# Kernel optimization log

Hardware: AMD Instinct MI355X
Metric: run time of the kernel (lower is better)

## Reference

```python
import jax, jax.numpy as jnp
import numpy as np

D_MODEL, D_INNER, D_STATE, D_CONV, DT_RANK = 192, 384, 16, 4, 12
EPS = 1e-5


def _causal_dwconv(x, w, b):
    # x: (B, L, Din); w: (Din, 1, K) depthwise; causal left pad K-1
    xc = x.transpose(0, 2, 1)  # (B, Din, L)
    y = jax.lax.conv_general_dilated(xc, w, window_strides=(1,),
                                     padding=[(D_CONV - 1, 0)],
                                     feature_group_count=D_INNER,
                                     dimension_numbers=('NCH', 'OIH', 'NCH'))
    return (y + b[None, :, None]).transpose(0, 2, 1)  # (B, L, Din)


def _ssm_dir(xh, z, conv_w, conv_b, x_proj_w, dt_w, dt_b, A_log, D):
    # one direction of the selective scan
    x = jax.nn.silu(_causal_dwconv(xh, conv_w, conv_b))  # (B, L, Din)
    x_dbl = jnp.einsum('bld,ed->ble', x, x_proj_w)       # (B, L, R+2N)
    dt = jax.nn.softplus(jnp.einsum('blr,dr->bld', x_dbl[..., :DT_RANK], dt_w) + dt_b)
    Bm = x_dbl[..., DT_RANK:DT_RANK + D_STATE]           # (B, L, N)
    Cm = x_dbl[..., DT_RANK + D_STATE:]                  # (B, L, N)
    A = -jnp.exp(A_log)                                  # (Din, N)
    deltaA = jnp.exp(dt[..., None] * A)                  # (B, L, Din, N)
    dBx = (dt * x)[..., None] * Bm[:, :, None, :]        # (B, L, Din, N)

    def comb(e1, e2):
        a1, b1 = e1
        a2, b2 = e2
        return a1 * a2, a2 * b1 + b2

    _, h = jax.lax.associative_scan(comb, (deltaA, dBx), axis=1)
    y = jnp.einsum('bldn,bln->bld', h, Cm) + x * D
    return y * jax.nn.silu(z)


def setup_inputs() -> dict:
    key = jax.random.key(0)
    ks = jax.random.split(key, 24)
    B, L = 2, 2048
    s = 0.02
    inp = {
        'hidden_states': jax.random.normal(ks[0], (B, L, D_MODEL), jnp.float32),
        'residual': jax.random.normal(ks[1], (B, L, D_MODEL), jnp.float32),
        'norm_w': jnp.ones((D_MODEL,), jnp.float32),
        'in_proj_w': jax.random.normal(ks[2], (2 * D_INNER, D_MODEL)) * s,
        'out_proj_w': jax.random.normal(ks[3], (D_MODEL, D_INNER)) * s,
        # forward-direction SSM params
        'conv_w_f': jax.random.normal(ks[4], (D_INNER, 1, D_CONV)) * s,
        'conv_b_f': jnp.zeros((D_INNER,), jnp.float32),
        'x_proj_w_f': jax.random.normal(ks[5], (DT_RANK + 2 * D_STATE, D_INNER)) * s,
        'dt_w_f': jax.random.normal(ks[6], (D_INNER, DT_RANK)) * s,
        'dt_b_f': jax.random.uniform(ks[7], (D_INNER,), minval=-4.0, maxval=-2.0),
        'A_log_f': jnp.log(jnp.tile(jnp.arange(1, D_STATE + 1, dtype=jnp.float32), (D_INNER, 1))),
        'D_f': jnp.ones((D_INNER,), jnp.float32),
        # backward-direction SSM params (bimamba)
        'conv_w_b': jax.random.normal(ks[8], (D_INNER, 1, D_CONV)) * s,
        'conv_b_b': jnp.zeros((D_INNER,), jnp.float32),
        'x_proj_w_b': jax.random.normal(ks[9], (DT_RANK + 2 * D_STATE, D_INNER)) * s,
        'dt_w_b': jax.random.normal(ks[10], (D_INNER, DT_RANK)) * s,
        'dt_b_b': jax.random.uniform(ks[11], (D_INNER,), minval=-4.0, maxval=-2.0),
        'A_log_b': jnp.log(jnp.tile(jnp.arange(1, D_STATE + 1, dtype=jnp.float32), (D_INNER, 1))),
        'D_b': jnp.ones((D_INNER,), jnp.float32),
    }
    return inp


def reference(hidden_states, residual, norm_w, in_proj_w, out_proj_w,
              conv_w_f, conv_b_f, x_proj_w_f, dt_w_f, dt_b_f, A_log_f, D_f,
              conv_w_b, conv_b_b, x_proj_w_b, dt_w_b, dt_b_b, A_log_b, D_b):
    # fused add + RMSNorm (prenorm=True): residual_out = hidden + residual (fp32)
    residual_out = (hidden_states + residual).astype(jnp.float32)
    x = residual_out * jax.lax.rsqrt(jnp.mean(residual_out * residual_out, axis=-1, keepdims=True) + EPS)
    x = x * norm_w
    # Mamba mixer, bimamba=True
    xz = jnp.einsum('bld,ed->ble', x, in_proj_w)  # (B, L, 2*Din)
    xh, z = xz[..., :D_INNER], xz[..., D_INNER:]
    y_f = _ssm_dir(xh, z, conv_w_f, conv_b_f, x_proj_w_f, dt_w_f, dt_b_f, A_log_f, D_f)
    y_b = _ssm_dir(xh[:, ::-1], z[:, ::-1], conv_w_b, conv_b_b, x_proj_w_b, dt_w_b, dt_b_b, A_log_b, D_b)[:, ::-1]
    out = jnp.einsum('bld,ed->ble', y_f + y_b, out_proj_w)
    return out, residual_out
```

## Files before the change

kernel.cpp:

```cpp
#include <hip/hip_runtime.h>
#include <math.h>

#define BB 2
#define LL 2048
#define DM 192
#define DI 384
#define DS 16
#define RK 12
#define NROW (BB*LL)
#define NCH 64
#define CLEN (LL/NCH)
#define EP 48

__device__ __forceinline__ float siluf(float v) { return v / (1.f + __expf(-v)); }

#define N_IN  (DM * 2 * DI)
#define N_OUT (DI * DM)
#define N_XP  (2 * DI * EP)
#define N_DT  (2 * RK * DI)
#define N_PREP (N_IN + N_OUT + N_XP + N_DT)

__global__ __launch_bounds__(256) void k_wprep(
    const float* __restrict__ wip, const float* __restrict__ wop,
    const float* __restrict__ xpwf, const float* __restrict__ xpwb,
    const float* __restrict__ dtwf, const float* __restrict__ dtwb,
    float* __restrict__ wt_in, float* __restrict__ wt_out,
    float* __restrict__ wt_xp, float* __restrict__ wt_dt) {
  int i = blockIdx.x * 256 + threadIdx.x;
  if (i < N_IN) {
    int k = i / (2 * DI), c = i % (2 * DI);
    wt_in[i] = wip[c * DM + k];
  } else if (i < N_IN + N_OUT) {
    int t = i - N_IN;
    int k = t / DM, c = t % DM;
    wt_out[t] = wop[c * DI + k];
  } else if (i < N_IN + N_OUT + N_XP) {
    int t = i - N_IN - N_OUT;
    int dir = t / (DI * EP), rem = t % (DI * EP);
    int k = rem / EP, e = rem % EP;
    const float* src = dir ? xpwb : xpwf;
    wt_xp[t] = (e < RK + 2 * DS) ? src[e * DI + k] : 0.f;
  } else if (i < N_PREP) {
    int t = i - N_IN - N_OUT - N_XP;
    int dir = t / (RK * DI), rem = t % (RK * DI);
    int j = rem / DI, d = rem % DI;
    const float* src = dir ? dtwb : dtwf;
    wt_dt[t] = src[d * RK + j];
  }
}

__global__ __launch_bounds__(256) void k_rmsnorm(
    const float* __restrict__ h, const float* __restrict__ r,
    const float* __restrict__ w, float* __restrict__ res, float* __restrict__ xn) {
  int row = blockIdx.x * 4 + (threadIdx.x >> 6);
  int lane = threadIdx.x & 63;
  const float* hp = h + row * DM;
  const float* rp = r + row * DM;
  float v0 = hp[lane]       + rp[lane];
  float v1 = hp[lane + 64]  + rp[lane + 64];
  float v2 = hp[lane + 128] + rp[lane + 128];
  float ss = v0 * v0 + v1 * v1 + v2 * v2;
  #pragma unroll
  for (int o = 32; o; o >>= 1) ss += __shfl_xor(ss, o);
  float inv = rsqrtf(ss * (1.f / DM) + 1e-5f);
  float* rr = res + row * DM;
  float* xo = xn + row * DM;
  rr[lane] = v0; rr[lane + 64] = v1; rr[lane + 128] = v2;
  xo[lane]       = v0 * inv * w[lane];
  xo[lane + 64]  = v1 * inv * w[lane + 64];
  xo[lane + 128] = v2 * inv * w[lane + 128];
}

__global__ __launch_bounds__(256) void k_inproj(
    const float* __restrict__ xn, const float* __restrict__ wt,
    float* __restrict__ xh, float* __restrict__ z) {
  __shared__ float xs[DM][16];
  int r0 = blockIdx.x * 16;
  int c = blockIdx.y * 256 + threadIdx.x;
  for (int idx = threadIdx.x; idx < 16 * DM; idx += 256) {
    int r = idx & 15, k = idx >> 4;
    xs[k][r] = xn[(r0 + r) * DM + k];
  }
  __syncthreads();
  const float* wc = wt + c;
  float acc[16];
  #pragma unroll
  for (int i = 0; i < 16; i++) acc[i] = 0.f;
  for (int k = 0; k < DM; k += 4) {
    float w0 = wc[(k+0) * (2*DI)];
    float w1 = wc[(k+1) * (2*DI)];
    float w2 = wc[(k+2) * (2*DI)];
    float w3 = wc[(k+3) * (2*DI)];
    float wv4[4] = {w0, w1, w2, w3};
    #pragma unroll
    for (int kk = 0; kk < 4; kk++) {
      float wv = wv4[kk];
      const float4* xr = reinterpret_cast<const float4*>(&xs[k + kk][0]);
      #pragma unroll
      for (int q = 0; q < 4; q++) {
        float4 a = xr[q];
        acc[4*q+0] += wv * a.x; acc[4*q+1] += wv * a.y;
        acc[4*q+2] += wv * a.z; acc[4*q+3] += wv * a.w;
      }
    }
  }
  float* dst = (c < DI) ? (xh + c) : (z + (c - DI));
  #pragma unroll
  for (int r2 = 0; r2 < 16; r2++) dst[(r0 + r2) * DI] = acc[r2];
}

__global__ __launch_bounds__(256) void k_conv(
    const float* __restrict__ xh,
    const float* __restrict__ cwf, const float* __restrict__ cbf,
    const float* __restrict__ cwb, const float* __restrict__ cbb,
    float* __restrict__ xc) {
  int dir = blockIdx.y;
  int g = blockIdx.x * 256 + threadIdx.x;
  int row = g / DI, d = g % DI;
  int b = row >> 11, s = row & (LL - 1);
  const float* cw = dir ? cwb : cwf;
  const float* cb = dir ? cbb : cbf;
  float acc = cb[d];
  #pragma unroll
  for (int k = 0; k < 4; k++) {
    int sp = s - 3 + k;
    if (sp >= 0) {
      int mr = b * LL + (dir ? (LL - 1 - sp) : sp);
      acc += cw[d * 4 + k] * xh[mr * DI + d];
    }
  }
  xc[(dir * NROW + row) * DI + d] = siluf(acc);
}

__global__ __launch_bounds__(256) void k_xproj(
    const float* __restrict__ xc,
    const float* __restrict__ wt_xp, const float* __restrict__ wt_dt,
    const float* __restrict__ dtbf, const float* __restrict__ dtbb,
    float* __restrict__ dt, float* __restrict__ Bm, float* __restrict__ Cm) {
  int dir = blockIdx.y;
  int r0 = blockIdx.x * 16;
  const float* wxp = wt_xp + dir * DI * EP;
  const float* wdt = wt_dt + dir * RK * DI;
  const float* dtb = dir ? dtbb : dtbf;
  __shared__ float xs[16][DI];
  __shared__ float xd[16][EP];
  for (int idx = threadIdx.x; idx < 16 * DI; idx += 256) {
    int r = idx / DI, d2 = idx % DI;
    xs[r][d2] = xc[(size_t)(dir * NROW + r0 + r) * DI + d2];
  }
  __syncthreads();
  for (int o = threadIdx.x; o < 16 * EP; o += 256) {
    int r = o / EP, e = o % EP;
    const float* wcol = wxp + e;
    const float4* xr = reinterpret_cast<const float4*>(&xs[r][0]);
    float ax = 0.f, ay = 0.f, az = 0.f, aw = 0.f;
    #pragma unroll 4
    for (int q = 0; q < DI / 4; q++) {
      float4 x = xr[q];
      ax += wcol[(4*q+0) * EP] * x.x;
      ay += wcol[(4*q+1) * EP] * x.y;
      az += wcol[(4*q+2) * EP] * x.z;
      aw += wcol[(4*q+3) * EP] * x.w;
    }
    xd[r][e] = (ax + ay) + (az + aw);
  }
  __syncthreads();
  for (int o = threadIdx.x; o < 16 * DI; o += 256) {
    int r = o / DI, d2 = o % DI;
    float a = dtb[d2];
    #pragma unroll
    for (int j = 0; j < RK; j++) a += xd[r][j] * wdt[j * DI + d2];
    a = (a > 20.f) ? a : log1pf(__expf(a));
    dt[(size_t)(dir * NROW + r0 + r) * DI + d2] = a;
  }
  for (int o = threadIdx.x; o < 16 * 32; o += 256) {
    int r = o / 32, j = o % 32;
    float v = xd[r][RK + j];
    if (j < DS) Bm[(size_t)(dir * NROW + r0 + r) * DS + j] = v;
    else        Cm[(size_t)(dir * NROW + r0 + r) * DS + (j - DS)] = v;
  }
}

__global__ __launch_bounds__(128) void k_scan1(
    const float* __restrict__ dt, const float* __restrict__ xc,
    const float* __restrict__ Bm,
    const float* __restrict__ Alf, const float* __restrict__ Alb,
    float* __restrict__ S, float* __restrict__ P) {
  int zb = blockIdx.z;
  int dir = zb >> 1;
  int d = blockIdx.x * 128 + threadIdx.x;
  int c = blockIdx.y;
  const float* Al = dir ? Alb : Alf;
  float Av[DS];
  {
    const float4* ap = reinterpret_cast<const float4*>(Al + d * DS);
    #pragma unroll
    for (int q = 0; q < 4; q++) {
      float4 a = ap[q];
      Av[4*q+0] = -__expf(a.x); Av[4*q+1] = -__expf(a.y);
      Av[4*q+2] = -__expf(a.z); Av[4*q+3] = -__expf(a.w);
    }
  }
  int rowbase = zb * LL + c * CLEN;
  const float4* Bp4 = reinterpret_cast<const float4*>(Bm + (size_t)rowbase * DS);
  float h[DS];
  #pragma unroll
  for (int n = 0; n < DS; n++) h[n] = 0.f;
  float sdt = 0.f;
  float dtv = dt[(size_t)rowbase * DI + d];
  float xv  = xc[(size_t)rowbase * DI + d];
  #pragma unroll 4
  for (int s = 0; s < CLEN; s++) {
    float dtn_ = 0.f, xn_ = 0.f;
    if (s + 1 < CLEN) {
      dtn_ = dt[(size_t)(rowbase + s + 1) * DI + d];
      xn_  = xc[(size_t)(rowbase + s + 1) * DI + d];
    }
    float4 B0 = Bp4[s*4+0], B1 = Bp4[s*4+1], B2 = Bp4[s*4+2], B3 = Bp4[s*4+3];
    float Bv[DS] = {B0.x,B0.y,B0.z,B0.w, B1.x,B1.y,B1.z,B1.w,
                    B2.x,B2.y,B2.z,B2.w, B3.x,B3.y,B3.z,B3.w};
    float dtx = dtv * xv;
    sdt += dtv;
    #pragma unroll
    for (int n = 0; n < DS; n++) {
      float dA = __expf(dtv * Av[n]);
      h[n] = __fmaf_rn(dA, h[n], dtx * Bv[n]);
    }
    dtv = dtn_; xv = xn_;
  }
  size_t base = ((size_t)(zb * NCH + c) * DI + d) * DS;
  float4* Sp = reinterpret_cast<float4*>(S + base);
  float4* Pp = reinterpret_cast<float4*>(P + base);
  #pragma unroll
  for (int q = 0; q < 4; q++) {
    Sp[q] = make_float4(h[4*q+0], h[4*q+1], h[4*q+2], h[4*q+3]);
    Pp[q] = make_float4(__expf(Av[4*q+0]*sdt), __expf(Av[4*q+1]*sdt),
                        __expf(Av[4*q+2]*sdt), __expf(Av[4*q+3]*sdt));
  }
}

__global__ __launch_bounds__(256) void k_scan2(
    float* __restrict__ S, const float* __restrict__ P) {
  int g = blockIdx.x * 256 + threadIdx.x;
  int zb = g / (DI * DS);
  int rem = g % (DI * DS);
  const int stride = DI * DS;
  size_t base = (size_t)zb * NCH * stride + rem;
  float carry = 0.f;
  for (int c0 = 0; c0 < NCH; c0 += 8) {
    float p8[8], s8[8];
    #pragma unroll
    for (int j = 0; j < 8; j++) {
      p8[j] = P[base + (size_t)(c0 + j) * stride];
      s8[j] = S[base + (size_t)(c0 + j) * stride];
    }
    #pragma unroll
    for (int j = 0; j < 8; j++) {
      S[base + (size_t)(c0 + j) * stride] = carry;
      carry = __fmaf_rn(p8[j], carry, s8[j]);
    }
  }
}

__global__ __launch_bounds__(128) void k_scan3(
    const float* __restrict__ dt, const float* __restrict__ xc,
    const float* __restrict__ Bm, const float* __restrict__ Cm,
    const float* __restrict__ z, const float* __restrict__ Hin,
    const float* __restrict__ Alf, const float* __restrict__ Alb,
    const float* __restrict__ Df, const float* __restrict__ Db,
    float* __restrict__ y) {
  int zb = blockIdx.z;
  int dir = zb >> 1, b = zb & 1;
  int d = blockIdx.x * 128 + threadIdx.x;
  int c = blockIdx.y;
  const float* Al = dir ? Alb : Alf;
  const float* Dp = dir ? Db : Df;
  float Av[DS];
  {
    const float4* ap = reinterpret_cast<const float4*>(Al + d * DS);
    #pragma unroll
    for (int q = 0; q < 4; q++) {
      float4 a = ap[q];
      Av[4*q+0] = -__expf(a.x); Av[4*q+1] = -__expf(a.y);
      Av[4*q+2] = -__expf(a.z); Av[4*q+3] = -__expf(a.w);
    }
  }
  float Dv = Dp[d];
  int rowbase = zb * LL + c * CLEN;
  const float4* Bp4 = reinterpret_cast<const float4*>(Bm + (size_t)rowbase * DS);
  const float4* Cp4 = reinterpret_cast<const float4*>(Cm + (size_t)rowbase * DS);
  size_t base = ((size_t)(zb * NCH + c) * DI + d) * DS;
  float h[DS];
  {
    const float4* hp = reinterpret_cast<const float4*>(Hin + base);
    #pragma unroll
    for (int q = 0; q < 4; q++) {
      float4 a = hp[q];
      h[4*q+0] = a.x; h[4*q+1] = a.y; h[4*q+2] = a.z; h[4*q+3] = a.w;
    }
  }
  float dtv = dt[(size_t)rowbase * DI + d];
  float xv  = xc[(size_t)rowbase * DI + d];
  #pragma unroll 4
  for (int s = 0; s < CLEN; s++) {
    float dtn_ = 0.f, xn_ = 0.f;
    if (s + 1 < CLEN) {
      dtn_ = dt[(size_t)(rowbase + s + 1) * DI + d];
      xn_  = xc[(size_t)(rowbase + s + 1) * DI + d];
    }
    float4 B0 = Bp4[s*4+0], B1 = Bp4[s*4+1], B2 = Bp4[s*4+2], B3 = Bp4[s*4+3];
    float Bv[DS] = {B0.x,B0.y,B0.z,B0.w, B1.x,B1.y,B1.z,B1.w,
                    B2.x,B2.y,B2.z,B2.w, B3.x,B3.y,B3.z,B3.w};
    float4 C0 = Cp4[s*4+0], C1 = Cp4[s*4+1], C2 = Cp4[s*4+2], C3 = Cp4[s*4+3];
    float Cv[DS] = {C0.x,C0.y,C0.z,C0.w, C1.x,C1.y,C1.z,C1.w,
                    C2.x,C2.y,C2.z,C2.w, C3.x,C3.y,C3.z,C3.w};
    float dtx = dtv * xv;
    float acc = xv * Dv;
    #pragma unroll
    for (int n = 0; n < DS; n++) {
      float dA = __expf(dtv * Av[n]);
      h[n] = __fmaf_rn(dA, h[n], dtx * Bv[n]);
      acc = __fmaf_rn(h[n], Cv[n], acc);
    }
    int sg = c * CLEN + s;
    int mr = b * LL + (dir ? (LL - 1 - sg) : sg);
    float zv = z[(size_t)mr * DI + d];
    y[(size_t)(rowbase + s) * DI + d] = acc * siluf(zv);
    dtv = dtn_; xv = xn_;
  }
}

__global__ __launch_bounds__(192) void k_outproj(
    const float* __restrict__ y, const float* __restrict__ wt,
    float* __restrict__ out) {
  __shared__ float ys[DI][8];
  int r0 = blockIdx.x * 8;
  for (int idx = threadIdx.x; idx < 8 * DI; idx += 192) {
    int r = idx & 7, k = idx >> 3;
    int row = r0 + r;
    int b = row >> 11, l = row & (LL - 1);
    float vf = y[(size_t)(b * LL + l) * DI + k];
    float vb = y[(size_t)((2 + b) * LL + (LL - 1 - l)) * DI + k];
    ys[k][r] = vf + vb;
  }
  __syncthreads();
  int c = threadIdx.x;
  const float* wc = wt + c;
  float acc[8];
  #pragma unroll
  for (int i = 0; i < 8; i++) acc[i] = 0.f;
  for (int k = 0; k < DI; k += 4) {
    float w0 = wc[(k+0) * DM];
    float w1 = wc[(k+1) * DM];
    float w2 = wc[(k+2) * DM];
    float w3 = wc[(k+3) * DM];
    float wv4[4] = {w0, w1, w2, w3};
    #pragma unroll
    for (int kk = 0; kk < 4; kk++) {
      float wv = wv4[kk];
      const float4* xr = reinterpret_cast<const float4*>(&ys[k + kk][0]);
      float4 a0 = xr[0], a1 = xr[1];
      acc[0] += wv * a0.x; acc[1] += wv * a0.y;
      acc[2] += wv * a0.z; acc[3] += wv * a0.w;
      acc[4] += wv * a1.x; acc[5] += wv * a1.y;
      acc[6] += wv * a1.z; acc[7] += wv * a1.w;
    }
  }
  #pragma unroll
  for (int r2 = 0; r2 < 8; r2++) out[(r0 + r2) * DM + c] = acc[r2];
}

extern "C" void kernel_launch(void* const* d_in, const int* in_sizes, int n_in,
                              void* d_out, int out_size, void* d_ws, size_t ws_size,
                              hipStream_t stream) {
  const float* hid  = (const float*)d_in[0];
  const float* res  = (const float*)d_in[1];
  const float* nw   = (const float*)d_in[2];
  const float* wip  = (const float*)d_in[3];
  const float* wop  = (const float*)d_in[4];
  const float* cwf  = (const float*)d_in[5];
  const float* cbf  = (const float*)d_in[6];
  const float* xpwf = (const float*)d_in[7];
  const float* dtwf = (const float*)d_in[8];
  const float* dtbf = (const float*)d_in[9];
  const float* Alf  = (const float*)d_in[10];
  const float* Df   = (const float*)d_in[11];
  const float* cwb  = (const float*)d_in[12];
  const float* cbb  = (const float*)d_in[13];
  const float* xpwb = (const float*)d_in[14];
  const float* dtwb = (const float*)d_in[15];
  const float* dtbb = (const float*)d_in[16];
  const float* Alb  = (const float*)d_in[17];
  const float* Db   = (const float*)d_in[18];

  float* out_p  = (float*)d_out;
  float* resid  = out_p + NROW * DM;

  float* ws = (float*)d_ws;
  float* xn  = ws;
  float* xh  = xn  + NROW * DM;
  float* zz  = xh  + NROW * DI;
  float* xc  = zz  + NROW * DI;
  float* dt  = xc  + 2 * NROW * DI;
  float* Bm  = dt  + 2 * NROW * DI;
  float* Cm  = Bm  + 2 * NROW * DS;
  float* yy  = Cm  + 2 * NROW * DS;
  float* S   = yy  + 2 * NROW * DI;
  float* P   = S   + 2 * BB * NCH * DI * DS;
  float* wt_in  = P     + 2 * BB * NCH * DI * DS;
  float* wt_out = wt_in  + N_IN;
  float* wt_xp  = wt_out + N_OUT;
  float* wt_dt  = wt_xp  + N_XP;

  k_wprep<<<(N_PREP + 255) / 256, 256, 0, stream>>>(wip, wop, xpwf, xpwb, dtwf, dtwb,
                                                    wt_in, wt_out, wt_xp, wt_dt);
  k_rmsnorm<<<NROW / 4, 256, 0, stream>>>(hid, res, nw, resid, xn);
  k_inproj<<<dim3(NROW / 16, 3), 256, 0, stream>>>(xn, wt_in, xh, zz);
  k_conv<<<dim3(NROW * DI / 256, 2), 256, 0, stream>>>(xh, cwf, cbf, cwb, cbb, xc);
  k_xproj<<<dim3(NROW / 16, 2), 256, 0, stream>>>(xc, wt_xp, wt_dt, dtbf, dtbb,
                                                  dt, Bm, Cm);
  k_scan1<<<dim3(DI / 128, NCH, 2 * BB), 128, 0, stream>>>(dt, xc, Bm, Alf, Alb, S, P);
  k_scan2<<<(2 * BB * DI * DS) / 256, 256, 0, stream>>>(S, P);
  k_scan3<<<dim3(DI / 128, NCH, 2 * BB), 128, 0, stream>>>(dt, xc, Bm, Cm, zz, S,
                                                           Alf, Alb, Df, Db, yy);
  k_outproj<<<NROW / 8, 192, 0, stream>>>(yy, wt_out, out_p);
}
```

Baseline: 258.1 us.

## Pack projection weights in k-quad interleaved layout for float4 loads

```diff
diff --git a/kernel.cpp b/kernel.cpp
--- a/kernel.cpp
+++ b/kernel.cpp
@@ -10,38 +10,40 @@
 #define NROW (BB*LL)
 #define NCH 64
 #define CLEN (LL/NCH)
-#define EP 48
+#define EQ 64
 
 __device__ __forceinline__ float siluf(float v) { return v / (1.f + __expf(-v)); }
 
 #define N_IN  (DM * 2 * DI)
 #define N_OUT (DI * DM)
-#define N_XP  (2 * DI * EP)
+#define N_XPQ (2 * (DI/4) * EQ * 4)
 #define N_DT  (2 * RK * DI)
-#define N_PREP (N_IN + N_OUT + N_XP + N_DT)
+#define N_PREP (N_IN + N_OUT + N_XPQ + N_DT)
 
 __global__ __launch_bounds__(256) void k_wprep(
     const float* __restrict__ wip, const float* __restrict__ wop,
     const float* __restrict__ xpwf, const float* __restrict__ xpwb,
     const float* __restrict__ dtwf, const float* __restrict__ dtwb,
-    float* __restrict__ wt_in, float* __restrict__ wt_out,
-    float* __restrict__ wt_xp, float* __restrict__ wt_dt) {
+    float* __restrict__ wq_in, float* __restrict__ wt_out,
+    float* __restrict__ wq_xp, float* __restrict__ wt_dt) {
   int i = blockIdx.x * 256 + threadIdx.x;
   if (i < N_IN) {
-    int k = i / (2 * DI), c = i % (2 * DI);
-    wt_in[i] = wip[c * DM + k];
+    int kq = i / (2 * DI * 4), rem = i % (2 * DI * 4);
+    int c = rem / 4, ii = rem % 4;
+    wq_in[i] = wip[c * DM + kq * 4 + ii];
   } else if (i < N_IN + N_OUT) {
     int t = i - N_IN;
     int k = t / DM, c = t % DM;
     wt_out[t] = wop[c * DI + k];
-  } else if (i < N_IN + N_OUT + N_XP) {
+  } else if (i < N_IN + N_OUT + N_XPQ) {
     int t = i - N_IN - N_OUT;
-    int dir = t / (DI * EP), rem = t % (DI * EP);
-    int k = rem / EP, e = rem % EP;
+    int dir = t / ((DI/4) * EQ * 4), rem = t % ((DI/4) * EQ * 4);
+    int kq = rem / (EQ * 4), rem2 = rem % (EQ * 4);
+    int e = rem2 / 4, ii = rem2 % 4;
     const float* src = dir ? xpwb : xpwf;
-    wt_xp[t] = (e < RK + 2 * DS) ? src[e * DI + k] : 0.f;
+    wq_xp[t] = (e < RK + 2 * DS) ? src[e * DI + kq * 4 + ii] : 0.f;
   } else if (i < N_PREP) {
-    int t = i - N_IN - N_OUT - N_XP;
+    int t = i - N_IN - N_OUT - N_XPQ;
     int dir = t / (RK * DI), rem = t % (RK * DI);
     int j = rem / DI, d = rem % DI;
     const float* src = dir ? dtwb : dtwf;
@@ -72,7 +74,7 @@
 }
 
 __global__ __launch_bounds__(256) void k_inproj(
-    const float* __restrict__ xn, const float* __restrict__ wt,
+    const float* __restrict__ xn, const float* __restrict__ wq,
     float* __restrict__ xh, float* __restrict__ z) {
   __shared__ float xs[DM][16];
   int r0 = blockIdx.x * 16;
@@ -82,25 +84,21 @@
     xs[k][r] = xn[(r0 + r) * DM + k];
   }
   __syncthreads();
-  const float* wc = wt + c;
   float acc[16];
   #pragma unroll
   for (int i = 0; i < 16; i++) acc[i] = 0.f;
-  for (int k = 0; k < DM; k += 4) {
-    float w0 = wc[(k+0) * (2*DI)];
-    float w1 = wc[(k+1) * (2*DI)];
-    float w2 = wc[(k+2) * (2*DI)];
-    float w3 = wc[(k+3) * (2*DI)];
-    float wv4[4] = {w0, w1, w2, w3};
+  for (int kq = 0; kq < DM / 4; kq++) {
+    float4 wv = *reinterpret_cast<const float4*>(wq + ((size_t)(kq * 2 * DI) + c) * 4);
+    float wv4[4] = {wv.x, wv.y, wv.z, wv.w};
     #pragma unroll
     for (int kk = 0; kk < 4; kk++) {
-      float wv = wv4[kk];
-      const float4* xr = reinterpret_cast<const float4*>(&xs[k + kk][0]);
+      float w = wv4[kk];
+      const float4* xr = reinterpret_cast<const float4*>(&xs[kq * 4 + kk][0]);
       #pragma unroll
       for (int q = 0; q < 4; q++) {
         float4 a = xr[q];
-        acc[4*q+0] += wv * a.x; acc[4*q+1] += wv * a.y;
-        acc[4*q+2] += wv * a.z; acc[4*q+3] += wv * a.w;
+        acc[4*q+0] += w * a.x; acc[4*q+1] += w * a.y;
+        acc[4*q+2] += w * a.z; acc[4*q+3] += w * a.w;
       }
     }
   }
@@ -132,40 +130,46 @@
   xc[(dir * NROW + row) * DI + d] = siluf(acc);
 }
 
-__global__ __launch_bounds__(256) void k_xproj(
+__global__ __launch_bounds__(128) void k_xproj(
     const float* __restrict__ xc,
-    const float* __restrict__ wt_xp, const float* __restrict__ wt_dt,
+    const float* __restrict__ wq_xp, const float* __restrict__ wt_dt,
     const float* __restrict__ dtbf, const float* __restrict__ dtbb,
     float* __restrict__ dt, float* __restrict__ Bm, float* __restrict__ Cm) {
   int dir = blockIdx.y;
-  int r0 = blockIdx.x * 16;
-  const float* wxp = wt_xp + dir * DI * EP;
+  int r0 = blockIdx.x * 8;
+  const float* wq  = wq_xp + (size_t)dir * (DI/4) * EQ * 4;
   const float* wdt = wt_dt + dir * RK * DI;
   const float* dtb = dir ? dtbb : dtbf;
-  __shared__ float xs[16][DI];
-  __shared__ float xd[16][EP];
-  for (int idx = threadIdx.x; idx < 16 * DI; idx += 256) {
-    int r = idx / DI, d2 = idx % DI;
-    xs[r][d2] = xc[(size_t)(dir * NROW + r0 + r) * DI + d2];
+  __shared__ float xs[8][DI];
+  __shared__ float xd[8][EQ];
+  for (int idx = threadIdx.x; idx < 8 * DI; idx += 128) {
+    int r = idx / DI, k = idx % DI;
+    xs[r][k] = xc[(size_t)(dir * NROW + r0 + r) * DI + k];
   }
   __syncthreads();
-  for (int o = threadIdx.x; o < 16 * EP; o += 256) {
-    int r = o / EP, e = o % EP;
-    const float* wcol = wxp + e;
-    const float4* xr = reinterpret_cast<const float4*>(&xs[r][0]);
-    float ax = 0.f, ay = 0.f, az = 0.f, aw = 0.f;
-    #pragma unroll 4
-    for (int q = 0; q < DI / 4; q++) {
-      float4 x = xr[q];
-      ax += wcol[(4*q+0) * EP] * x.x;
-      ay += wcol[(4*q+1) * EP] * x.y;
-      az += wcol[(4*q+2) * EP] * x.z;
-      aw += wcol[(4*q+3) * EP] * x.w;
-    }
-    xd[r][e] = (ax + ay) + (az + aw);
+  {
+    int e  = threadIdx.x & 63;
+    int rg = threadIdx.x >> 6;
+    float a0 = 0.f, a1 = 0.f, a2 = 0.f, a3 = 0.f;
+    #pragma unroll 2
+    for (int kq = 0; kq < DI / 4; kq++) {
+      float4 wv = *reinterpret_cast<const float4*>(wq + ((kq << 6) + e) * 4);
+      float4 x0 = *reinterpret_cast<const float4*>(&xs[rg * 4 + 0][kq * 4]);
+      float4 x1 = *reinterpret_cast<const float4*>(&xs[rg * 4 + 1][kq * 4]);
+      float4 x2 = *reinterpret_cast<const float4*>(&xs[rg * 4 + 2][kq * 4]);
+      float4 x3 = *reinterpret_cast<const float4*>(&xs[rg * 4 + 3][kq * 4]);
+      a0 += wv.x * x0.x + wv.y * x0.y + wv.z * x0.z + wv.w * x0.w;
+      a1 += wv.x * x1.x + wv.y * x1.y + wv.z * x1.z + wv.w * x1.w;
+      a2 += wv.x * x2.x + wv.y * x2.y + wv.z * x2.z + wv.w * x2.w;
+      a3 += wv.x * x3.x + wv.y * x3.y + wv.z * x3.z + wv.w * x3.w;
+    }
+    xd[rg * 4 + 0][e] = a0;
+    xd[rg * 4 + 1][e] = a1;
+    xd[rg * 4 + 2][e] = a2;
+    xd[rg * 4 + 3][e] = a3;
   }
   __syncthreads();
-  for (int o = threadIdx.x; o < 16 * DI; o += 256) {
+  for (int o = threadIdx.x; o < 8 * DI; o += 128) {
     int r = o / DI, d2 = o % DI;
     float a = dtb[d2];
     #pragma unroll
@@ -173,7 +177,7 @@
     a = (a > 20.f) ? a : log1pf(__expf(a));
     dt[(size_t)(dir * NROW + r0 + r) * DI + d2] = a;
   }
-  for (int o = threadIdx.x; o < 16 * 32; o += 256) {
+  for (int o = threadIdx.x; o < 8 * 32; o += 128) {
     int r = o / 32, j = o % 32;
     float v = xd[r][RK + j];
     if (j < DS) Bm[(size_t)(dir * NROW + r0 + r) * DS + j] = v;
@@ -407,18 +411,18 @@
   float* yy  = Cm  + 2 * NROW * DS;
   float* S   = yy  + 2 * NROW * DI;
   float* P   = S   + 2 * BB * NCH * DI * DS;
-  float* wt_in  = P     + 2 * BB * NCH * DI * DS;
-  float* wt_out = wt_in  + N_IN;
-  float* wt_xp  = wt_out + N_OUT;
-  float* wt_dt  = wt_xp  + N_XP;
+  float* wq_in  = P     + 2 * BB * NCH * DI * DS;
+  float* wt_out = wq_in  + N_IN;
+  float* wq_xp  = wt_out + N_OUT;
+  float* wt_dt  = wq_xp  + N_XPQ;
 
   k_wprep<<<(N_PREP + 255) / 256, 256, 0, stream>>>(wip, wop, xpwf, xpwb, dtwf, dtwb,
-                                                    wt_in, wt_out, wt_xp, wt_dt);
+                                                    wq_in, wt_out, wq_xp, wt_dt);
   k_rmsnorm<<<NROW / 4, 256, 0, stream>>>(hid, res, nw, resid, xn);
-  k_inproj<<<dim3(NROW / 16, 3), 256, 0, stream>>>(xn, wt_in, xh, zz);
+  k_inproj<<<dim3(NROW / 16, 3), 256, 0, stream>>>(xn, wq_in, xh, zz);
   k_conv<<<dim3(NROW * DI / 256, 2), 256, 0, stream>>>(xh, cwf, cbf, cwb, cbb, xc);
-  k_xproj<<<dim3(NROW / 16, 2), 256, 0, stream>>>(xc, wt_xp, wt_dt, dtbf, dtbb,
-                                                  dt, Bm, Cm);
+  k_xproj<<<dim3(NROW / 8, 2), 128, 0, stream>>>(xc, wq_xp, wt_dt, dtbf, dtbb,
+                                                 dt, Bm, Cm);
   k_scan1<<<dim3(DI / 128, NCH, 2 * BB), 128, 0, stream>>>(dt, xc, Bm, Alf, Alb, S, P);
   k_scan2<<<(2 * BB * DI * DS) / 256, 256, 0, stream>>>(S, P);
   k_scan3<<<dim3(DI / 128, NCH, 2 * BB), 128, 0, stream>>>(dt, xc, Bm, Cm, zz, S,
```

After: 260.2 us. Within noise of the previous version (+0.8%).
